# Optimization experiments

Measured on AMD Instinct MI355X. Metric: run time of the kernel, lower is better.

The kernel has to match this reference:

```python
import jax, jax.numpy as jnp
import numpy as np
from math import sqrt

B, T, E, W, H = 4, 512, 1024, 64, 16
DK = E // H


def _make_position_mask(T, W):
    # mask[s, w, t] = 1 iff token s is the w-th neighbor in the window around t
    t = np.arange(T)[None, :]            # [1, T]
    w = np.arange(W)[:, None]            # [W, 1]
    idx = np.clip(t - W // 2 + w, 0, T - 1)  # [W, T] source index per (w, t)
    mask = np.zeros((T, W, T), dtype=np.float32)
    mask[idx, np.arange(W)[:, None], np.arange(T)[None, :]] = 1.0
    return jnp.asarray(mask)


def setup_inputs() -> dict:
    key = jax.random.key(0)
    ks = jax.random.split(key, 7)
    s = 1.0 / sqrt(E)
    return {
        "x": jax.random.normal(ks[0], (B, T, E), jnp.float32),
        "position_mask": _make_position_mask(T, W),
        "Wq": jax.random.normal(ks[1], (E, E), jnp.float32) * s,
        "bq": jnp.zeros((E,), jnp.float32),
        "Wv": jax.random.normal(ks[2], (E, E), jnp.float32) * s,
        "bv": jnp.zeros((E,), jnp.float32),
        "Wo": jax.random.normal(ks[3], (E, E), jnp.float32) * s,
        "bo": jnp.zeros((E,), jnp.float32),
    }


def reference(x, position_mask, Wq, bq, Wv, bv, Wo, bo):
    # gather window neighbors: attend_inputs[b,t,w,e] = sum_s x[b,s,e] * mask[s,w,t]
    attend = jnp.einsum('bse,swt->btwe', x, position_mask)  # [B,T,W,E]

    # NOTE: original splits E as (d_k, H) with d_k-major (view(..., d_k, H))
    q = (x @ Wq + bq).reshape(B, T, DK, H)                    # [B,T,DK,H]
    q = q.transpose(0, 3, 1, 2)                               # [B,H,T,DK]
    k = (attend @ Wq + bq).reshape(B, T, W, DK, H)            # key uses query_transform (as in source)
    k = k.transpose(0, 4, 1, 2, 3)                            # [B,H,T,W,DK]
    v = (attend @ Wv + bv).reshape(B, T, W, DK, H)
    v = v.transpose(0, 4, 1, 2, 3)                            # [B,H,T,W,DK]

    scores = jnp.einsum('bhtd,bhtwd->bhtw', q, k) / sqrt(E)   # scale by sqrt(E), as in source
    probs = jax.nn.softmax(scores, axis=-1)                   # softmax over window W
    out = jnp.einsum('bhtw,bhtwd->bhtd', probs, v)            # [B,H,T,DK]
    out = out.transpose(0, 2, 1, 3).reshape(B, T, E)          # merge (H, DK) H-major, as in source reshape
    return out @ Wo + bo
```

## Files before the change

### kernel.cpp

```cpp
#include <hip/hip_runtime.h>
#include <hip/hip_bf16.h>

typedef __attribute__((ext_vector_type(8))) short short8;
typedef __attribute__((ext_vector_type(4))) float f32x4;
typedef __attribute__((ext_vector_type(4))) unsigned int uint4v;

constexpr int NB = 4, NT = 512, NE = 1024, NW = 64, NH = 16, NDK = 64;
constexpr int NBT = NB * NT;
constexpr int TT = 32;
constexpr int WIN = TT + 64;

__device__ inline short f2bf(float f) {
    __hip_bfloat16 h = __float2bfloat16(f);
    return __builtin_bit_cast(short, h);
}
__device__ inline float bf2f(short s) {
    unsigned u = ((unsigned)(unsigned short)s) << 16;
    return __builtin_bit_cast(float, u);
}
__device__ inline float blo(unsigned u) { return __builtin_bit_cast(float, u << 16); }
__device__ inline float bhi(unsigned u) { return __builtin_bit_cast(float, u & 0xffff0000u); }

__global__ __launch_bounds__(256) void cast_x_kernel(const float* __restrict__ X,
                                                     short* __restrict__ Xb) {
    size_t idx = (size_t)blockIdx.x * 256 + threadIdx.x;
    const float4* p = (const float4*)(X + idx * 8);
    float4 a = p[0], b = p[1];
    short8 v;
    v[0] = f2bf(a.x); v[1] = f2bf(a.y); v[2] = f2bf(a.z); v[3] = f2bf(a.w);
    v[4] = f2bf(b.x); v[5] = f2bf(b.y); v[6] = f2bf(b.z); v[7] = f2bf(b.w);
    *(short8*)(Xb + idx * 8) = v;
}

__global__ __launch_bounds__(256) void transpose_w_kernel(const float* __restrict__ W0,
                                                          const float* __restrict__ W1,
                                                          const float* __restrict__ W2,
                                                          short* __restrict__ WTall) {
    const float* W = blockIdx.z == 0 ? W0 : (blockIdx.z == 1 ? W1 : W2);
    const bool perm = blockIdx.z < 2;
    short* WT = WTall + (size_t)blockIdx.z * NE * NE;

    __shared__ float tile[64][65];
    const int e0 = blockIdx.y * 64, j0 = blockIdx.x * 64;
    const int el = threadIdx.x & 63, grp = threadIdx.x >> 6;
    for (int i = grp; i < 64; i += 4)
        tile[i][el] = W[(size_t)(e0 + i) * NE + j0 + el];
    __syncthreads();
    for (int it = grp; it < 64; it += 4) {
        int j = j0 + it;
        int jp = perm ? ((j & 15) * 64 + (j >> 4)) : j;
        WT[(size_t)jp * NE + e0 + el] = f2bf(tile[el][it]);
    }
}

template <int BM, int BN, int LOG_GX, bool PERM_BIAS, bool OUT_BF16, bool DUAL>
__global__ __launch_bounds__(256) void mfma_gemm_kernel(const short* __restrict__ X,
                                                        const short* __restrict__ WT,
                                                        const float* __restrict__ bias0,
                                                        const float* __restrict__ bias1,
                                                        void* __restrict__ out0,
                                                        void* __restrict__ out1) {
    constexpr int MR = BM / 32, NR = BN / 32;
    constexpr int RDA = BM / 32, RDB = BN / 32;

    __shared__ short As[BM * 64];
    __shared__ short Bs[BN * 64];
    const int tid = threadIdx.x;
    const int lane = tid & 63, wid = tid >> 6;

    const int nwg = (1 << LOG_GX) * gridDim.y;
    const int bid = blockIdx.y * (1 << LOG_GX) + blockIdx.x;
    const int swz = (bid & 7) * (nwg >> 3) + (bid >> 3);
    const int r0 = (swz >> LOG_GX) * BM;
    const int c0 = (swz & ((1 << LOG_GX) - 1)) * BN;
    const int wr = (wid >> 1) * (BM / 2), wc = (wid & 1) * (BN / 2);

    f32x4 acc[MR][NR];
#pragma unroll
    for (int m = 0; m < MR; m++)
#pragma unroll
        for (int n = 0; n < NR; n++) acc[m][n] = (f32x4){0.f, 0.f, 0.f, 0.f};

    short8 pfA[RDA], pfB[RDB];
    auto load_tiles = [&](int k0) {
#pragma unroll
        for (int rd = 0; rd < RDA; rd++) {
            int slot = rd * 4096 + tid * 16;
            int row  = slot >> 7;
            int c    = ((slot >> 4) & 7) ^ (row & 7);
            pfA[rd] = *(const short8*)(X + (size_t)(r0 + row) * NE + k0 + c * 8);
        }
#pragma unroll
        for (int rd = 0; rd < RDB; rd++) {
            int slot = rd * 4096 + tid * 16;
            int row  = slot >> 7;
            int c    = ((slot >> 4) & 7) ^ (row & 7);
            pfB[rd] = *(const short8*)(WT + (size_t)(c0 + row) * NE + k0 + c * 8);
        }
    };

    load_tiles(0);
    for (int k0 = 0; k0 < NE; k0 += 64) {
        __syncthreads();
#pragma unroll
        for (int rd = 0; rd < RDA; rd++)
            *(short8*)((char*)As + rd * 4096 + tid * 16) = pfA[rd];
#pragma unroll
        for (int rd = 0; rd < RDB; rd++)
            *(short8*)((char*)Bs + rd * 4096 + tid * 16) = pfB[rd];
        __syncthreads();
        if (k0 + 64 < NE) load_tiles(k0 + 64);

#pragma unroll
        for (int kk = 0; kk < 2; kk++) {
            short8 af[MR], bf[NR];
            const int cidx = kk * 4 + (lane >> 4);
#pragma unroll
            for (int m = 0; m < MR; m++) {
                int row = wr + m * 16 + (lane & 15);
                af[m] = *(const short8*)((char*)As + row * 128 + ((cidx ^ (row & 7)) * 16));
            }
#pragma unroll
            for (int n = 0; n < NR; n++) {
                int row = wc + n * 16 + (lane & 15);
                bf[n] = *(const short8*)((char*)Bs + row * 128 + ((cidx ^ (row & 7)) * 16));
            }
#pragma unroll
            for (int m = 0; m < MR; m++)
#pragma unroll
                for (int n = 0; n < NR; n++)
                    acc[m][n] = __builtin_amdgcn_mfma_f32_16x16x32_bf16(af[m], bf[n], acc[m][n], 0, 0, 0);
        }
    }

    const float* bias = bias0;
    void* outv = out0;
    int cbase = c0;
    if (DUAL && c0 >= NE) { bias = bias1; outv = out1; cbase = c0 - NE; }
    short* outS = (short*)outv;
    float* outF = (float*)outv;
#pragma unroll
    for (int m = 0; m < MR; m++)
#pragma unroll
        for (int n = 0; n < NR; n++) {
            int lc   = cbase + wc + n * 16 + (lane & 15);
            int bsrc = PERM_BIAS ? ((lc & 63) * 16 + (lc >> 6)) : lc;
            float bb = bias[bsrc];
#pragma unroll
            for (int r = 0; r < 4; r++) {
                int row = r0 + wr + m * 16 + (lane >> 4) * 4 + r;
                float val = acc[m][n][r] + bb;
                if (OUT_BF16) outS[(size_t)row * NE + lc] = f2bf(val);
                else          outF[(size_t)row * NE + lc] = val;
            }
        }
}

__global__ __launch_bounds__(256) void attn_kernel(const short* __restrict__ Y,
                                                   const short* __restrict__ Z,
                                                   short* __restrict__ M) {
    __shared__ short KS[WIN][66];
    __shared__ short VS[WIN][66];
    __shared__ short SCb[TT][66];
    __shared__ float RED[TT][16];

    const int t0 = blockIdx.x * TT;
    const int h  = blockIdx.y;
    const int b  = blockIdx.z;
    const int tid = threadIdx.x;
    const int tl  = tid & (TT - 1);
    const int oct = tid >> 5;

    for (int idx = tid; idx < WIN * 8; idx += 256) {
        int row = idx >> 3, c = idx & 7;
        int ts = t0 - 32 + row;
        ts = ts < 0 ? 0 : (ts > NT - 1 ? NT - 1 : ts);
        size_t base = ((size_t)b * NT + ts) * NE + h * 64 + c * 8;
        uint4v ku = __builtin_bit_cast(uint4v, *(const short8*)(Y + base));
        uint4v vu = __builtin_bit_cast(uint4v, *(const short8*)(Z + base));
        unsigned* kd = (unsigned*)&KS[row][c * 8];
        unsigned* vd = (unsigned*)&VS[row][c * 8];
        kd[0] = ku[0]; kd[1] = ku[1]; kd[2] = ku[2]; kd[3] = ku[3];
        vd[0] = vu[0]; vd[1] = vu[1]; vd[2] = vu[2]; vd[3] = vu[3];
    }
    __syncthreads();

    float q[64];
    {
        const unsigned* Qr = (const unsigned*)&KS[tl + 32][0];
#pragma unroll
        for (int k2 = 0; k2 < 32; k2++) {
            unsigned u = Qr[k2];
            q[2 * k2]     = blo(u);
            q[2 * k2 + 1] = bhi(u);
        }
    }

    float sv[8];
#pragma unroll
    for (int wi = 0; wi < 8; wi++) {
        int w = oct * 8 + wi;
        const unsigned* Kr = (const unsigned*)&KS[tl + w][0];
        float acc = 0.f;
#pragma unroll
        for (int k2 = 0; k2 < 32; k2++) {
            unsigned u = Kr[k2];
            acc += q[2 * k2] * blo(u) + q[2 * k2 + 1] * bhi(u);
        }
        sv[wi] = acc * 0.03125f;
    }

    float lmax = sv[0];
#pragma unroll
    for (int wi = 1; wi < 8; wi++) lmax = fmaxf(lmax, sv[wi]);
    RED[tl][oct] = lmax;
    __syncthreads();
    float gmax = RED[tl][0];
#pragma unroll
    for (int i = 1; i < 8; i++) gmax = fmaxf(gmax, RED[tl][i]);
    float lsum = 0.f;
#pragma unroll
    for (int wi = 0; wi < 8; wi++) {
        float e = __expf(sv[wi] - gmax);
        SCb[tl][oct * 8 + wi] = f2bf(e);
        lsum += e;
    }
    RED[tl][8 + oct] = lsum;
    __syncthreads();
    float gsum = RED[tl][8];
#pragma unroll
    for (int i = 9; i < 16; i++) gsum += RED[tl][i];

    float oacc[8];
#pragma unroll
    for (int j = 0; j < 8; j++) oacc[j] = 0.f;
    for (int w = 0; w < NW; w++) {
        float p = bf2f(SCb[tl][w]);
        const unsigned* Vr = (const unsigned*)&VS[tl + w][oct * 8];
#pragma unroll
        for (int j2 = 0; j2 < 4; j2++) {
            unsigned u = Vr[j2];
            oacc[2 * j2]     += p * blo(u);
            oacc[2 * j2 + 1] += p * bhi(u);
        }
    }

    float inv = 1.0f / gsum;
    short8 ov;
#pragma unroll
    for (int j = 0; j < 8; j++) ov[j] = f2bf(oacc[j] * inv);
    size_t orow = ((size_t)b * NT + t0 + tl) * NE + h * 64 + oct * 8;
    *(short8*)(M + orow) = ov;
}

extern "C" void kernel_launch(void* const* d_in, const int* in_sizes, int n_in,
                              void* d_out, int out_size, void* d_ws, size_t ws_size,
                              hipStream_t stream) {
    const float* x  = (const float*)d_in[0];
    const float* Wq = (const float*)d_in[2];
    const float* bq = (const float*)d_in[3];
    const float* Wv = (const float*)d_in[4];
    const float* bv = (const float*)d_in[5];
    const float* Wo = (const float*)d_in[6];
    const float* bo = (const float*)d_in[7];
    float* outp = (float*)d_out;

    char* wsb = (char*)d_ws;
    short* Xb  = (short*)(wsb);
    short* WTa = (short*)(wsb + (4u << 20));
    short* Yb  = (short*)(wsb + (10u << 20));
    short* Zb  = (short*)(wsb + (14u << 20));
    short* Mb  = (short*)(wsb + (18u << 20));
    short* WTo = WTa + 2 * (size_t)NE * NE;

    cast_x_kernel<<<dim3(NBT * NE / (256 * 8)), 256, 0, stream>>>(x, Xb);
    transpose_w_kernel<<<dim3(16, 16, 3), 256, 0, stream>>>(Wq, Wv, Wo, WTa);

    mfma_gemm_kernel<128, 128, 4, true, true, true>
        <<<dim3(2 * NE / 128, NBT / 128), 256, 0, stream>>>(Xb, WTa, bq, bv, Yb, Zb);

    attn_kernel<<<dim3(NT / TT, NH, NB), 256, 0, stream>>>(Yb, Zb, Mb);

    mfma_gemm_kernel<64, 128, 3, false, false, false>
        <<<dim3(NE / 128, NBT / 64), 256, 0, stream>>>(Mb, WTo, bo, nullptr, (void*)outp, nullptr);
}
```

Measured before the change: 168.8 us.

## Use MFMA for windowed attention, fuse x cast into GEMM, store V transposed

The scalar attention kernel is replaced by one that computes the QK scores and the PV product with bf16 MFMA tiles. It also swizzles K in shared memory, and V arrives pre-transposed from the projection GEMM through a swapped MFMA operand order and a transposed store. The separate fp32-to-bf16 cast of x is folded into the GEMM's A-tile load, removing one kernel and one round trip through workspace. The cost is extra MFMA work on the full 32x96 tile, including entries outside the band, plus strided transposed stores in the V epilogue.

```diff
diff --git a/kernel.cpp b/kernel.cpp
--- a/kernel.cpp
+++ b/kernel.cpp
@@ -3,33 +3,14 @@
 
 typedef __attribute__((ext_vector_type(8))) short short8;
 typedef __attribute__((ext_vector_type(4))) float f32x4;
-typedef __attribute__((ext_vector_type(4))) unsigned int uint4v;
-
-constexpr int NB = 4, NT = 512, NE = 1024, NW = 64, NH = 16, NDK = 64;
-constexpr int NBT = NB * NT;
+
+constexpr int NB = 4, NT = 512, NE = 1024, NH = 16;
+constexpr int NBT = 2048;
 constexpr int TT = 32;
-constexpr int WIN = TT + 64;
 
 __device__ inline short f2bf(float f) {
     __hip_bfloat16 h = __float2bfloat16(f);
     return __builtin_bit_cast(short, h);
-}
-__device__ inline float bf2f(short s) {
-    unsigned u = ((unsigned)(unsigned short)s) << 16;
-    return __builtin_bit_cast(float, u);
-}
-__device__ inline float blo(unsigned u) { return __builtin_bit_cast(float, u << 16); }
-__device__ inline float bhi(unsigned u) { return __builtin_bit_cast(float, u & 0xffff0000u); }
-
-__global__ __launch_bounds__(256) void cast_x_kernel(const float* __restrict__ X,
-                                                     short* __restrict__ Xb) {
-    size_t idx = (size_t)blockIdx.x * 256 + threadIdx.x;
-    const float4* p = (const float4*)(X + idx * 8);
-    float4 a = p[0], b = p[1];
-    short8 v;
-    v[0] = f2bf(a.x); v[1] = f2bf(a.y); v[2] = f2bf(a.z); v[3] = f2bf(a.w);
-    v[4] = f2bf(b.x); v[5] = f2bf(b.y); v[6] = f2bf(b.z); v[7] = f2bf(b.w);
-    *(short8*)(Xb + idx * 8) = v;
 }
 
 __global__ __launch_bounds__(256) void transpose_w_kernel(const float* __restrict__ W0,
@@ -53,16 +34,14 @@
     }
 }
 
-template <int BM, int BN, int LOG_GX, bool PERM_BIAS, bool OUT_BF16, bool DUAL>
-__global__ __launch_bounds__(256) void mfma_gemm_kernel(const short* __restrict__ X,
+template <int BM, int BN, int LOG_GX, bool A_F32, bool ZT_DUAL, bool PERM_BIAS, bool OUT_BF16>
+__global__ __launch_bounds__(256) void mfma_gemm_kernel(const void* __restrict__ Xv,
                                                         const short* __restrict__ WT,
                                                         const float* __restrict__ bias0,
                                                         const float* __restrict__ bias1,
                                                         void* __restrict__ out0,
-                                                        void* __restrict__ out1) {
+                                                        short* __restrict__ outZt) {
     constexpr int MR = BM / 32, NR = BN / 32;
-    constexpr int RDA = BM / 32, RDB = BN / 32;
-
     __shared__ short As[BM * 64];
     __shared__ short Bs[BN * 64];
     const int tid = threadIdx.x;
@@ -74,6 +53,7 @@
     const int r0 = (swz >> LOG_GX) * BM;
     const int c0 = (swz & ((1 << LOG_GX) - 1)) * BN;
     const int wr = (wid >> 1) * (BM / 2), wc = (wid & 1) * (BN / 2);
+    const bool isZ = ZT_DUAL && (c0 >= NE);
 
     f32x4 acc[MR][NR];
 #pragma unroll
@@ -81,17 +61,26 @@
 #pragma unroll
         for (int n = 0; n < NR; n++) acc[m][n] = (f32x4){0.f, 0.f, 0.f, 0.f};
 
-    short8 pfA[RDA], pfB[RDB];
+    short8 pfA[MR], pfB[NR];
     auto load_tiles = [&](int k0) {
 #pragma unroll
-        for (int rd = 0; rd < RDA; rd++) {
+        for (int rd = 0; rd < MR; rd++) {
             int slot = rd * 4096 + tid * 16;
             int row  = slot >> 7;
             int c    = ((slot >> 4) & 7) ^ (row & 7);
-            pfA[rd] = *(const short8*)(X + (size_t)(r0 + row) * NE + k0 + c * 8);
-        }
-#pragma unroll
-        for (int rd = 0; rd < RDB; rd++) {
+            if (A_F32) {
+                const float* xa = (const float*)Xv + (size_t)(r0 + row) * NE + k0 + c * 8;
+                float4 a = *(const float4*)xa, b = *(const float4*)(xa + 4);
+                short8 v;
+                v[0] = f2bf(a.x); v[1] = f2bf(a.y); v[2] = f2bf(a.z); v[3] = f2bf(a.w);
+                v[4] = f2bf(b.x); v[5] = f2bf(b.y); v[6] = f2bf(b.z); v[7] = f2bf(b.w);
+                pfA[rd] = v;
+            } else {
+                pfA[rd] = *(const short8*)((const short*)Xv + (size_t)(r0 + row) * NE + k0 + c * 8);
+            }
+        }
+#pragma unroll
+        for (int rd = 0; rd < NR; rd++) {
             int slot = rd * 4096 + tid * 16;
             int row  = slot >> 7;
             int c    = ((slot >> 4) & 7) ^ (row & 7);
@@ -103,10 +92,10 @@
     for (int k0 = 0; k0 < NE; k0 += 64) {
         __syncthreads();
 #pragma unroll
-        for (int rd = 0; rd < RDA; rd++)
+        for (int rd = 0; rd < MR; rd++)
             *(short8*)((char*)As + rd * 4096 + tid * 16) = pfA[rd];
 #pragma unroll
-        for (int rd = 0; rd < RDB; rd++)
+        for (int rd = 0; rd < NR; rd++)
             *(short8*)((char*)Bs + rd * 4096 + tid * 16) = pfB[rd];
         __syncthreads();
         if (k0 + 64 < NE) load_tiles(k0 + 64);
@@ -125,132 +114,186 @@
                 int row = wc + n * 16 + (lane & 15);
                 bf[n] = *(const short8*)((char*)Bs + row * 128 + ((cidx ^ (row & 7)) * 16));
             }
-#pragma unroll
-            for (int m = 0; m < MR; m++)
-#pragma unroll
-                for (int n = 0; n < NR; n++)
-                    acc[m][n] = __builtin_amdgcn_mfma_f32_16x16x32_bf16(af[m], bf[n], acc[m][n], 0, 0, 0);
-        }
-    }
-
-    const float* bias = bias0;
-    void* outv = out0;
-    int cbase = c0;
-    if (DUAL && c0 >= NE) { bias = bias1; outv = out1; cbase = c0 - NE; }
-    short* outS = (short*)outv;
-    float* outF = (float*)outv;
-#pragma unroll
-    for (int m = 0; m < MR; m++)
-#pragma unroll
-        for (int n = 0; n < NR; n++) {
-            int lc   = cbase + wc + n * 16 + (lane & 15);
-            int bsrc = PERM_BIAS ? ((lc & 63) * 16 + (lc >> 6)) : lc;
-            float bb = bias[bsrc];
-#pragma unroll
-            for (int r = 0; r < 4; r++) {
-                int row = r0 + wr + m * 16 + (lane >> 4) * 4 + r;
-                float val = acc[m][n][r] + bb;
-                if (OUT_BF16) outS[(size_t)row * NE + lc] = f2bf(val);
-                else          outF[(size_t)row * NE + lc] = val;
-            }
-        }
-}
-
-__global__ __launch_bounds__(256) void attn_kernel(const short* __restrict__ Y,
-                                                   const short* __restrict__ Z,
-                                                   short* __restrict__ M) {
-    __shared__ short KS[WIN][66];
-    __shared__ short VS[WIN][66];
-    __shared__ short SCb[TT][66];
-    __shared__ float RED[TT][16];
+            if (isZ) {
+#pragma unroll
+                for (int m = 0; m < MR; m++)
+#pragma unroll
+                    for (int n = 0; n < NR; n++)
+                        acc[m][n] = __builtin_amdgcn_mfma_f32_16x16x32_bf16(bf[n], af[m], acc[m][n], 0, 0, 0);
+            } else {
+#pragma unroll
+                for (int m = 0; m < MR; m++)
+#pragma unroll
+                    for (int n = 0; n < NR; n++)
+                        acc[m][n] = __builtin_amdgcn_mfma_f32_16x16x32_bf16(af[m], bf[n], acc[m][n], 0, 0, 0);
+            }
+        }
+    }
+
+    if (isZ) {
+        const int cb = c0 - NE;
+        const int tok = r0 + wr + (lane & 15);
+#pragma unroll
+        for (int m = 0; m < MR; m++)
+#pragma unroll
+            for (int n = 0; n < NR; n++)
+#pragma unroll
+                for (int r = 0; r < 4; r++) {
+                    int jp = cb + wc + n * 16 + (lane >> 4) * 4 + r;
+                    float bb = bias1[(jp & 63) * 16 + (jp >> 6)];
+                    outZt[(size_t)jp * NBT + tok + m * 16] = f2bf(acc[m][n][r] + bb);
+                }
+    } else {
+        short* outS = (short*)out0;
+        float* outF = (float*)out0;
+#pragma unroll
+        for (int m = 0; m < MR; m++)
+#pragma unroll
+            for (int n = 0; n < NR; n++) {
+                int lc   = c0 + wc + n * 16 + (lane & 15);
+                int bsrc = PERM_BIAS ? ((lc & 63) * 16 + (lc >> 6)) : lc;
+                float bb = bias0[bsrc];
+#pragma unroll
+                for (int r = 0; r < 4; r++) {
+                    int row = r0 + wr + m * 16 + (lane >> 4) * 4 + r;
+                    float val = acc[m][n][r] + bb;
+                    if (OUT_BF16) outS[(size_t)row * NE + lc] = f2bf(val);
+                    else          outF[(size_t)row * NE + lc] = val;
+                }
+            }
+    }
+}
+
+__global__ __launch_bounds__(256) void attn_kernel(const short* __restrict__ Yb,
+                                                   const short* __restrict__ Zt,
+                                                   short* __restrict__ Mb) {
+    __shared__ __align__(16) short KS[96][64];
+    __shared__ __align__(16) short VT[64][96];
+    __shared__ __align__(16) float SL[32][100];
+    __shared__ __align__(16) short PL[32][104];
+    __shared__ float RED[32][17];
 
     const int t0 = blockIdx.x * TT;
     const int h  = blockIdx.y;
     const int b  = blockIdx.z;
     const int tid = threadIdx.x;
-    const int tl  = tid & (TT - 1);
-    const int oct = tid >> 5;
-
-    for (int idx = tid; idx < WIN * 8; idx += 256) {
-        int row = idx >> 3, c = idx & 7;
-        int ts = t0 - 32 + row;
+    const int lane = tid & 63, wid = tid >> 6;
+
+    for (int u = tid; u < 416; u += 256)
+        *(short8*)((short*)PL + u * 8) = (short8){0, 0, 0, 0, 0, 0, 0, 0};
+
+    for (int u = tid; u < 768; u += 256) {
+        int r = u >> 3, c = u & 7;
+        int ts = t0 - 32 + r;
         ts = ts < 0 ? 0 : (ts > NT - 1 ? NT - 1 : ts);
-        size_t base = ((size_t)b * NT + ts) * NE + h * 64 + c * 8;
-        uint4v ku = __builtin_bit_cast(uint4v, *(const short8*)(Y + base));
-        uint4v vu = __builtin_bit_cast(uint4v, *(const short8*)(Z + base));
-        unsigned* kd = (unsigned*)&KS[row][c * 8];
-        unsigned* vd = (unsigned*)&VS[row][c * 8];
-        kd[0] = ku[0]; kd[1] = ku[1]; kd[2] = ku[2]; kd[3] = ku[3];
-        vd[0] = vu[0]; vd[1] = vu[1]; vd[2] = vu[2]; vd[3] = vu[3];
+        short8 kv = *(const short8*)(Yb + ((size_t)b * NT + ts) * NE + h * 64 + c * 8);
+        *(short8*)&KS[r][(c ^ (r & 7)) * 8] = kv;
+    }
+    {
+        const int d = tid >> 2, cbase = (tid & 3) * 3;
+        const short* zr = Zt + (size_t)(h * 64 + d) * NBT + b * NT;
+#pragma unroll
+        for (int i = 0; i < 3; i++) {
+            int ch = cbase + i;
+            int s0 = t0 - 32 + ch * 8;
+            short8 v;
+            if (s0 >= 0 && s0 <= NT - 8) {
+                v = *(const short8*)(zr + s0);
+            } else {
+#pragma unroll
+                for (int j = 0; j < 8; j++) {
+                    int ss = s0 + j;
+                    ss = ss < 0 ? 0 : (ss > NT - 1 ? NT - 1 : ss);
+                    v[j] = zr[ss];
+                }
+            }
+            *(short8*)&VT[d][ch * 8] = v;
+        }
     }
     __syncthreads();
 
-    float q[64];
     {
-        const unsigned* Qr = (const unsigned*)&KS[tl + 32][0];
-#pragma unroll
-        for (int k2 = 0; k2 < 32; k2++) {
-            unsigned u = Qr[k2];
-            q[2 * k2]     = blo(u);
-            q[2 * k2 + 1] = bhi(u);
-        }
-    }
-
-    float sv[8];
-#pragma unroll
-    for (int wi = 0; wi < 8; wi++) {
-        int w = oct * 8 + wi;
-        const unsigned* Kr = (const unsigned*)&KS[tl + w][0];
-        float acc = 0.f;
-#pragma unroll
-        for (int k2 = 0; k2 < 32; k2++) {
-            unsigned u = Kr[k2];
-            acc += q[2 * k2] * blo(u) + q[2 * k2 + 1] * bhi(u);
-        }
-        sv[wi] = acc * 0.03125f;
-    }
-
-    float lmax = sv[0];
-#pragma unroll
-    for (int wi = 1; wi < 8; wi++) lmax = fmaxf(lmax, sv[wi]);
-    RED[tl][oct] = lmax;
+        const int mq = wid >> 1, ntrio = (wid & 1) * 3;
+        f32x4 sacc[3];
+#pragma unroll
+        for (int ni = 0; ni < 3; ni++) sacc[ni] = (f32x4){0.f, 0.f, 0.f, 0.f};
+#pragma unroll
+        for (int ks = 0; ks < 2; ks++) {
+            const int cidx = ks * 4 + (lane >> 4);
+            int qrow = 32 + mq * 16 + (lane & 15);
+            short8 af = *(const short8*)((char*)KS + qrow * 128 + ((cidx ^ (qrow & 7)) * 16));
+#pragma unroll
+            for (int ni = 0; ni < 3; ni++) {
+                int srow = (ntrio + ni) * 16 + (lane & 15);
+                short8 bf = *(const short8*)((char*)KS + srow * 128 + ((cidx ^ (srow & 7)) * 16));
+                sacc[ni] = __builtin_amdgcn_mfma_f32_16x16x32_bf16(af, bf, sacc[ni], 0, 0, 0);
+            }
+        }
+#pragma unroll
+        for (int ni = 0; ni < 3; ni++)
+#pragma unroll
+            for (int r = 0; r < 4; r++)
+                SL[mq * 16 + (lane >> 4) * 4 + r][(ntrio + ni) * 16 + (lane & 15)] =
+                    sacc[ni][r] * 0.03125f;
+    }
     __syncthreads();
-    float gmax = RED[tl][0];
-#pragma unroll
-    for (int i = 1; i < 8; i++) gmax = fmaxf(gmax, RED[tl][i]);
-    float lsum = 0.f;
-#pragma unroll
-    for (int wi = 0; wi < 8; wi++) {
-        float e = __expf(sv[wi] - gmax);
-        SCb[tl][oct * 8 + wi] = f2bf(e);
-        lsum += e;
-    }
-    RED[tl][8 + oct] = lsum;
+
+    {
+        const int tl = tid & (TT - 1), oct = tid >> 5;
+        float sv[8];
+#pragma unroll
+        for (int wi = 0; wi < 8; wi++) sv[wi] = SL[tl][tl + oct * 8 + wi];
+        float lmax = sv[0];
+#pragma unroll
+        for (int wi = 1; wi < 8; wi++) lmax = fmaxf(lmax, sv[wi]);
+        RED[tl][oct] = lmax;
+        __syncthreads();
+        float gmax = RED[tl][0];
+#pragma unroll
+        for (int i = 1; i < 8; i++) gmax = fmaxf(gmax, RED[tl][i]);
+        float lsum = 0.f;
+#pragma unroll
+        for (int wi = 0; wi < 8; wi++) {
+            float e = __expf(sv[wi] - gmax);
+            PL[tl][tl + oct * 8 + wi] = f2bf(e);
+            lsum += e;
+        }
+        RED[tl][8 + oct] = lsum;
+        __syncthreads();
+        float gsum = RED[tl][8];
+#pragma unroll
+        for (int i = 9; i < 16; i++) gsum += RED[tl][i];
+        if (oct == 0) RED[tl][16] = 1.0f / gsum;
+    }
     __syncthreads();
-    float gsum = RED[tl][8];
-#pragma unroll
-    for (int i = 9; i < 16; i++) gsum += RED[tl][i];
-
-    float oacc[8];
-#pragma unroll
-    for (int j = 0; j < 8; j++) oacc[j] = 0.f;
-    for (int w = 0; w < NW; w++) {
-        float p = bf2f(SCb[tl][w]);
-        const unsigned* Vr = (const unsigned*)&VS[tl + w][oct * 8];
-#pragma unroll
-        for (int j2 = 0; j2 < 4; j2++) {
-            unsigned u = Vr[j2];
-            oacc[2 * j2]     += p * blo(u);
-            oacc[2 * j2 + 1] += p * bhi(u);
-        }
-    }
-
-    float inv = 1.0f / gsum;
-    short8 ov;
-#pragma unroll
-    for (int j = 0; j < 8; j++) ov[j] = f2bf(oacc[j] * inv);
-    size_t orow = ((size_t)b * NT + t0 + tl) * NE + h * 64 + oct * 8;
-    *(short8*)(M + orow) = ov;
+
+    {
+        const int mp = wid >> 1, npair = (wid & 1) * 2;
+        f32x4 oacc[2];
+#pragma unroll
+        for (int ni = 0; ni < 2; ni++) oacc[ni] = (f32x4){0.f, 0.f, 0.f, 0.f};
+#pragma unroll
+        for (int ks = 0; ks < 3; ks++) {
+            int prow = mp * 16 + (lane & 15);
+            short8 pa = *(const short8*)((char*)PL + prow * 208 + ks * 64 + (lane >> 4) * 16);
+#pragma unroll
+            for (int ni = 0; ni < 2; ni++) {
+                int d = (npair + ni) * 16 + (lane & 15);
+                short8 bv = *(const short8*)((char*)VT + d * 192 + ks * 64 + (lane >> 4) * 16);
+                oacc[ni] = __builtin_amdgcn_mfma_f32_16x16x32_bf16(pa, bv, oacc[ni], 0, 0, 0);
+            }
+        }
+#pragma unroll
+        for (int ni = 0; ni < 2; ni++) {
+            int d = (npair + ni) * 16 + (lane & 15);
+#pragma unroll
+            for (int r = 0; r < 4; r++) {
+                int tl = mp * 16 + (lane >> 4) * 4 + r;
+                float inv = RED[tl][16];
+                Mb[((size_t)b * NT + t0 + tl) * NE + h * 64 + d] = f2bf(oacc[ni][r] * inv);
+            }
+        }
+    }
 }
 
 extern "C" void kernel_launch(void* const* d_in, const int* in_sizes, int n_in,
@@ -266,21 +309,19 @@
     float* outp = (float*)d_out;
 
     char* wsb = (char*)d_ws;
-    short* Xb  = (short*)(wsb);
-    short* WTa = (short*)(wsb + (4u << 20));
-    short* Yb  = (short*)(wsb + (10u << 20));
-    short* Zb  = (short*)(wsb + (14u << 20));
-    short* Mb  = (short*)(wsb + (18u << 20));
+    short* WTa = (short*)(wsb);
+    short* Yb  = (short*)(wsb + (6u << 20));
+    short* Zt  = (short*)(wsb + (10u << 20));
+    short* Mb  = (short*)(wsb + (14u << 20));
     short* WTo = WTa + 2 * (size_t)NE * NE;
 
-    cast_x_kernel<<<dim3(NBT * NE / (256 * 8)), 256, 0, stream>>>(x, Xb);
     transpose_w_kernel<<<dim3(16, 16, 3), 256, 0, stream>>>(Wq, Wv, Wo, WTa);
 
-    mfma_gemm_kernel<128, 128, 4, true, true, true>
-        <<<dim3(2 * NE / 128, NBT / 128), 256, 0, stream>>>(Xb, WTa, bq, bv, Yb, Zb);
-
-    attn_kernel<<<dim3(NT / TT, NH, NB), 256, 0, stream>>>(Yb, Zb, Mb);
-
-    mfma_gemm_kernel<64, 128, 3, false, false, false>
+    mfma_gemm_kernel<128, 128, 4, true, true, true, true>
+        <<<dim3(2 * NE / 128, NBT / 128), 256, 0, stream>>>(x, WTa, bq, bv, Yb, Zt);
+
+    attn_kernel<<<dim3(NT / TT, NH, NB), 256, 0, stream>>>(Yb, Zt, Mb);
+
+    mfma_gemm_kernel<64, 128, 3, false, false, false, false>
         <<<dim3(NE / 128, NBT / 64), 256, 0, stream>>>(Mb, WTo, bo, nullptr, (void*)outp, nullptr);
 }
```

New measurement: 171.1 us. About the same (+1.4%).
